# Performance work log

Measured on AMD Instinct MI355X. Metric: run time of the kernel, lower is better.

The kernel has to match this reference:

```python
import jax, jax.numpy as jnp
import numpy as np

HIDDEN = 1024
MOE_INTER = 512
SHARED_INTER = 2048
N_EXPERTS = 32
TOP_K = 6
N_GROUP = 8
TOPK_GROUP = 4
ROUTED_SCALE = 2.5


def setup_inputs() -> dict:
    key = jax.random.key(0)
    ks = jax.random.split(key, 6)
    s = 0.02
    return {
        "hidden_states": jax.random.normal(ks[0], (2, 1024, HIDDEN), jnp.float32),
        "gate_w": jax.random.normal(ks[1], (N_EXPERTS, HIDDEN), jnp.float32) * s,
        "e_bias": jnp.zeros((N_EXPERTS,), jnp.float32),  # e_score_correction_bias (non-trainable)
        "up_w": jax.random.normal(ks[2], (N_EXPERTS, MOE_INTER, HIDDEN), jnp.float32) * s,
        "down_w": jax.random.normal(ks[3], (N_EXPERTS, HIDDEN, MOE_INTER), jnp.float32) * s,
        "shared_up_w": jax.random.normal(ks[4], (SHARED_INTER, HIDDEN), jnp.float32) * s,
        "shared_down_w": jax.random.normal(ks[5], (HIDDEN, SHARED_INTER), jnp.float32) * s,
    }


def _relu2(x):
    # Nemotron-H 'relu2' activation: relu(x)^2
    return jnp.square(jax.nn.relu(x))


def _router(x, gate_w, e_bias):
    # x: [T, H] -> topk_idx [T, K] (int), topk_w [T, K] (fp32)
    T = x.shape[0]
    logits = x.astype(jnp.float32) @ gate_w.astype(jnp.float32).T  # [T, E]
    scores = jax.nn.sigmoid(logits)
    sc = scores + e_bias[None, :]
    # group-limited routing: top-2 sum per group, keep topk_group groups
    g = sc.reshape(T, N_GROUP, N_EXPERTS // N_GROUP)
    group_scores = jax.lax.top_k(g, 2)[0].sum(-1)                  # [T, G]
    group_idx = jax.lax.top_k(group_scores, TOPK_GROUP)[1]         # [T, TG]
    group_mask = jnp.zeros_like(group_scores).at[jnp.arange(T)[:, None], group_idx].set(1.0)
    score_mask = jnp.repeat(group_mask, N_EXPERTS // N_GROUP, axis=1)  # [T, E]
    masked = jnp.where(score_mask > 0, sc, 0.0)
    topk_idx = jax.lax.stop_gradient(jax.lax.top_k(masked, TOP_K)[1])  # torch path is @no_grad
    topk_w = jnp.take_along_axis(scores, topk_idx, axis=1)         # gather from unbiased scores
    topk_w = topk_w / (topk_w.sum(-1, keepdims=True) + 1e-20)      # norm_topk_prob
    topk_w = topk_w * ROUTED_SCALE
    return topk_idx, topk_w


def reference(hidden_states, gate_w, e_bias, up_w, down_w, shared_up_w, shared_down_w):
    B, S, H = hidden_states.shape
    x = hidden_states.reshape(-1, H)  # [T, H]
    T = x.shape[0]
    topk_idx, topk_w = _router(x, gate_w, e_bias)
    # combine weights as dense [T, E] (scatter of top-k weights)
    combine = jnp.zeros((T, N_EXPERTS), topk_w.dtype).at[jnp.arange(T)[:, None], topk_idx].add(topk_w)
    # dense-masked expert compute; weight applied on intermediate (equivalent since
    # down_proj is linear with no bias): out = sum_e w_te * down_e(act(up_e(x)))
    h = _relu2(jnp.einsum('th,eih->tei', x, up_w))   # [T, E, I]
    h = h * combine[:, :, None]
    moe_out = jnp.einsum('tei,ehi->th', h, down_w)   # [T, H]
    shared = _relu2(x @ shared_up_w.T) @ shared_down_w.T
    return (moe_out + shared).reshape(B, S, H)


if __name__ == "__main__":
    out = reference(**setup_inputs())
    print(out.shape, out.dtype)
```

## Files before the change

### kernel.cpp

```cpp
#include <hip/hip_runtime.h>

typedef unsigned short u16;
typedef __bf16 bf16x8 __attribute__((ext_vector_type(8)));
typedef float f32x4 __attribute__((ext_vector_type(4)));

#define T_TOK 2048
#define HID   1024
#define NEXP  32
#define IM    512
#define SI    2048
#define TOPK  6
#define PLAN_MAX 160

__device__ __forceinline__ u16 f2bf(float f){
  unsigned u = __float_as_uint(f);
  u += 0x7FFFu + ((u >> 16) & 1u);
  return (u16)(u >> 16);
}

__device__ __forceinline__ void gll16(const void* g, void* l){
  __builtin_amdgcn_global_load_lds((const __attribute__((address_space(1))) void*)g,
                                   (__attribute__((address_space(3))) void*)l, 16, 0, 0);
}

__global__ __launch_bounds__(256) void cvt_all_kernel(const float4* __restrict__ s0,
                                                      const float4* __restrict__ s1,
                                                      const float4* __restrict__ s2,
                                                      const float4* __restrict__ s3,
                                                      const float4* __restrict__ s4,
                                                      ushort4* __restrict__ d0,
                                                      ushort4* __restrict__ d1,
                                                      ushort4* __restrict__ d2,
                                                      ushort4* __restrict__ d3,
                                                      ushort4* __restrict__ d4){
  long i = (long)blockIdx.x * 256 + threadIdx.x;
  const float4* s; ushort4* d;
  if      (i <  524288L)                 { s = s0;            d = d0;            }
  else if (i <  524288L + 4194304L)      { s = s1 - 524288L;  d = d1 - 524288L;  }
  else if (i <  524288L + 8388608L)      { s = s2 - 4718592L; d = d2 - 4718592L; }
  else if (i <  524288L + 8912896L)      { s = s3 - 8912896L; d = d3 - 8912896L; }
  else                                   { s = s4 - 9437184L; d = d4 - 9437184L; }
  float4 v = s[i];
  ushort4 o; o.x = f2bf(v.x); o.y = f2bf(v.y); o.z = f2bf(v.z); o.w = f2bf(v.w);
  d[i] = o;
}

__global__ __launch_bounds__(256) void router_kernel(const float* __restrict__ x,
                                                     const float* __restrict__ gate,
                                                     const float* __restrict__ ebias,
                                                     int* __restrict__ ce,
                                                     float* __restrict__ cw){
  int wave = threadIdx.x >> 6;
  int lane = threadIdx.x & 63;
  int t = blockIdx.x * 4 + wave;
  int e = lane & 31, half = lane >> 5;
  const float4* xv = (const float4*)(x + (size_t)t * HID);
  const float4* gv = (const float4*)(gate + (size_t)e * HID);
  double d0 = 0, d1 = 0, d2 = 0, d3 = 0;
  for (int i = half * 128; i < half * 128 + 128; i++){
    float4 a = xv[i], b = gv[i];
    d0 += (double)a.x * b.x; d1 += (double)a.y * b.y;
    d2 += (double)a.z * b.z; d3 += (double)a.w * b.w;
  }
  double acc = (d0 + d1) + (d2 + d3);
  acc += __shfl_xor(acc, 32);
  double score = 1.0 / (1.0 + exp(-acc));
  double sc = score + (double)ebias[e];
  double o1  = __shfl_xor(sc, 1);
  double hi  = fmax(sc, o1), lo = fmin(sc, o1);
  double ohi = __shfl_xor(hi, 2), olo = __shfl_xor(lo, 2);
  double gs  = (hi >= ohi) ? hi + fmax(lo, ohi) : ohi + fmax(olo, hi);
  int g = e >> 2;
  int rank = 0;
#pragma unroll
  for (int j = 0; j < 8; j++){
    double gj = __shfl(gs, j * 4);
    if (gj > gs || (gj == gs && j < g)) rank++;
  }
  double cur = (rank < 4) ? sc : 0.0;
  int sel_e[TOPK]; double sel_w[TOPK]; double wsum = 0.0;
#pragma unroll
  for (int k = 0; k < TOPK; k++){
    double bv = cur; int bi = lane;
#pragma unroll
    for (int m = 32; m >= 1; m >>= 1){
      double ov = __shfl_xor(bv, m); int oi = __shfl_xor(bi, m);
      if (ov > bv || (ov == bv && oi < bi)) { bv = ov; bi = oi; }
    }
    if ((bi & 31) == e) cur = -1e300;
    double ws = __shfl(score, bi);
    sel_e[k] = bi; sel_w[k] = ws; wsum += ws;
  }
  double scale = 2.5 / (wsum + 1e-20);
#pragma unroll
  for (int k = 0; k < TOPK; k++){
    if (lane == k){
      ce[t * TOPK + k] = sel_e[k] & 31;
      cw[t * TOPK + k] = (float)(sel_w[k] * scale);
    }
  }
}

__global__ __launch_bounds__(256) void build_kernel(const int* __restrict__ ce,
                                                    const float* __restrict__ cw,
                                                    int* __restrict__ cnt,
                                                    int* __restrict__ tok,
                                                    float* __restrict__ wl){
  int e = blockIdx.x;
  int tid = threadIdx.x, lane = tid & 63, wave = tid >> 6;
  __shared__ int wsum[4];
  int running = 0;
  for (int base = 0; base < T_TOK * TOPK; base += 256){
    int i = base + tid;
    bool m = (ce[i] == e);
    unsigned long long bal = __ballot(m);
    int woff = __popcll(bal & ((1ull << lane) - 1ull));
    if (lane == 0) wsum[wave] = __popcll(bal);
    __syncthreads();
    int wbase = 0;
#pragma unroll
    for (int wv = 0; wv < 4; wv++) if (wv < wave) wbase += wsum[wv];
    int btot = wsum[0] + wsum[1] + wsum[2] + wsum[3];
    if (m){
      int t = i / TOPK, k = i - t * TOPK;
      int pos = running + wbase + woff;
      tok[e * T_TOK + pos] = (t << 3) | k;
      wl[e * T_TOK + pos] = cw[i];
    }
    running += btot;
    __syncthreads();
  }
  if (tid == 0) cnt[e] = running;
}

__global__ __launch_bounds__(256) void plan_kernel(const int* __restrict__ cnt,
                                                   int* __restrict__ plan){
  int tid = threadIdx.x;
  if (tid < PLAN_MAX) plan[1 + tid] = -1;
  __syncthreads();
  if (tid == 0){
    int n = 0;
    for (int e = 0; e < NEXP; e++){
      int c = cnt[e];
      for (int tb = 0; tb < c; tb += 128) plan[1 + n++] = (tb << 8) | e;
    }
    plan[0] = n;
  }
}

__device__ __forceinline__ void gemm_core(
    const char* gA0, const char* gA1, const char* gB0, const char* gB1,
    u16* lA, u16* lB, int iters, int tid, int wrow, int wcol, int quad, int l16,
    f32x4 acc[4][4])
{
  char* dA0 = (char*)lA + tid*16;
  char* dA1 = (char*)lA + 4096 + tid*16;
  char* dB0 = (char*)lB + tid*16;
  char* dB1 = (char*)lB + 4096 + tid*16;
  for (int it = 0; it < iters; ++it){
    gll16(gA0, dA0); gll16(gA1, dA1);
    gll16(gB0, dB0); gll16(gB1, dB1);
    gA0 += 64; gA1 += 64; gB0 += 64; gB1 += 64;
    __syncthreads();
    bf16x8 af[4], bfr[4];
#pragma unroll
    for (int mt = 0; mt < 4; mt++) af[mt] = *(const bf16x8*)&lA[(wrow + mt*16 + l16)*32 + quad*8];
#pragma unroll
    for (int nt = 0; nt < 4; nt++) bfr[nt] = *(const bf16x8*)&lB[(wcol + nt*16 + l16)*32 + quad*8];
#pragma unroll
    for (int mt = 0; mt < 4; mt++)
#pragma unroll
      for (int nt = 0; nt < 4; nt++)
        acc[mt][nt] = __builtin_amdgcn_mfma_f32_16x16x32_bf16(af[mt], bfr[nt], acc[mt][nt], 0, 0, 0);
    __syncthreads();
  }
}

#define ACC_INIT f32x4 acc[4][4]; \
  _Pragma("unroll") for (int i_ = 0; i_ < 4; i_++) \
  _Pragma("unroll") for (int j_ = 0; j_ < 4; j_++) acc[i_][j_] = (f32x4){0.f,0.f,0.f,0.f};

__global__ __launch_bounds__(256) void sh_up_kernel(const u16* __restrict__ A,
                                                    const u16* __restrict__ B,
                                                    u16* __restrict__ C){
  __shared__ u16 lA[128*32], lB[128*32];
  int tid = threadIdx.x;
  int bm = blockIdx.x*128, bn = blockIdx.y*128;
  int lane = tid & 63, wave = tid >> 6, quad = lane >> 4, l16 = lane & 15;
  int wrow = (wave >> 1)*64, wcol = (wave & 1)*64;
  int srow = tid >> 2, sseg = (tid & 3)*16;
  const char* gA0 = (const char*)(A + (size_t)(bm + srow)*HID) + sseg;
  const char* gA1 = (const char*)(A + (size_t)(bm + 64 + srow)*HID) + sseg;
  const char* gB0 = (const char*)(B + (size_t)(bn + srow)*HID) + sseg;
  const char* gB1 = (const char*)(B + (size_t)(bn + 64 + srow)*HID) + sseg;
  ACC_INIT;
  gemm_core(gA0, gA1, gB0, gB1, lA, lB, HID/32, tid, wrow, wcol, quad, l16, acc);
#pragma unroll
  for (int mt = 0; mt < 4; mt++)
#pragma unroll
    for (int nt = 0; nt < 4; nt++)
#pragma unroll
      for (int r = 0; r < 4; r++){
        int m = bm + wrow + mt*16 + quad*4 + r;
        int n = bn + wcol + nt*16 + l16;
        float v = acc[mt][nt][r]; v = fmaxf(v, 0.f); v *= v;
        C[(size_t)m*SI + n] = f2bf(v);
      }
}

__global__ __launch_bounds__(256) void sh_down_kernel(const u16* __restrict__ A,
                                                      const u16* __restrict__ B,
                                                      float* __restrict__ C){
  __shared__ u16 lA[128*32], lB[128*32];
  int tid = threadIdx.x;
  int bm = blockIdx.x*128, bn = blockIdx.y*128;
  int lane = tid & 63, wave = tid >> 6, quad = lane >> 4, l16 = lane & 15;
  int wrow = (wave >> 1)*64, wcol = (wave & 1)*64;
  int srow = tid >> 2, sseg = (tid & 3)*16;
  const char* gA0 = (const char*)(A + (size_t)(bm + srow)*SI) + sseg;
  const char* gA1 = (const char*)(A + (size_t)(bm + 64 + srow)*SI) + sseg;
  const char* gB0 = (const char*)(B + (size_t)(bn + srow)*SI) + sseg;
  const char* gB1 = (const char*)(B + (size_t)(bn + 64 + srow)*SI) + sseg;
  ACC_INIT;
  gemm_core(gA0, gA1, gB0, gB1, lA, lB, SI/32, tid, wrow, wcol, quad, l16, acc);
#pragma unroll
  for (int mt = 0; mt < 4; mt++)
#pragma unroll
    for (int nt = 0; nt < 4; nt++)
#pragma unroll
      for (int r = 0; r < 4; r++){
        int m = bm + wrow + mt*16 + quad*4 + r;
        int n = bn + wcol + nt*16 + l16;
        C[(size_t)m*HID + n] = acc[mt][nt][r];
      }
}

__global__ __launch_bounds__(256) void expert_up_kernel(const u16* __restrict__ xb,
                                                        const u16* __restrict__ upb,
                                                        const int* __restrict__ cnt,
                                                        const int* __restrict__ tok,
                                                        const float* __restrict__ wl,
                                                        const int* __restrict__ plan,
                                                        u16* __restrict__ hws){
  int pv = plan[1 + blockIdx.x];
  if (pv < 0) return;
  int e = pv & 255;
  int tb = pv >> 8;
  int c = cnt[e];
  int bn = blockIdx.y * 128;
  const int* tl = tok + e * T_TOK;
  const float* wle = wl + e * T_TOK;
  __shared__ u16 lA[128*32], lB[128*32];
  int tid = threadIdx.x;
  int lane = tid & 63, wave = tid >> 6, quad = lane >> 4, l16 = lane & 15;
  int wrow = (wave >> 1)*64, wcol = (wave & 1)*64;
  int srow = tid >> 2, sseg = (tid & 3)*16;
  int s0 = tb + srow;      if (s0 > c-1) s0 = c-1;
  int s1 = tb + 64 + srow; if (s1 > c-1) s1 = c-1;
  int t0 = tl[s0] >> 3, t1 = tl[s1] >> 3;
  const char* gA0 = (const char*)(xb + (size_t)t0*HID) + sseg;
  const char* gA1 = (const char*)(xb + (size_t)t1*HID) + sseg;
  const u16* Bb = upb + (size_t)e * IM * HID;
  const char* gB0 = (const char*)(Bb + (size_t)(bn + srow)*HID) + sseg;
  const char* gB1 = (const char*)(Bb + (size_t)(bn + 64 + srow)*HID) + sseg;
  ACC_INIT;
  gemm_core(gA0, gA1, gB0, gB1, lA, lB, HID/32, tid, wrow, wcol, quad, l16, acc);
#pragma unroll
  for (int mt = 0; mt < 4; mt++)
#pragma unroll
    for (int r = 0; r < 4; r++){
      int s = tb + wrow + mt*16 + quad*4 + r;
      if (s < c){
        int code = tl[s];
        float w = wle[s];
        size_t hb = ((size_t)(code >> 3) * TOPK + (code & 7)) * IM;
#pragma unroll
        for (int nt = 0; nt < 4; nt++){
          float v = acc[mt][nt][r]; v = fmaxf(v, 0.f); v = v * v * w;
          hws[hb + bn + wcol + nt*16 + l16] = f2bf(v);
        }
      }
    }
}

__global__ __launch_bounds__(256) void expert_down_kernel(const u16* __restrict__ hws,
                                                          const u16* __restrict__ dnb,
                                                          const int* __restrict__ cnt,
                                                          const int* __restrict__ tok,
                                                          const int* __restrict__ plan,
                                                          float* __restrict__ dws){
  int pv = plan[1 + blockIdx.x];
  if (pv < 0) return;
  int e = pv & 255;
  int tb = pv >> 8;
  int c = cnt[e];
  int bn = blockIdx.y * 128;
  const int* tl = tok + e * T_TOK;
  __shared__ u16 lA[128*32], lB[128*32];
  int tid = threadIdx.x;
  int lane = tid & 63, wave = tid >> 6, quad = lane >> 4, l16 = lane & 15;
  int wrow = (wave >> 1)*64, wcol = (wave & 1)*64;
  int srow = tid >> 2, sseg = (tid & 3)*16;
  int s0 = tb + srow;      if (s0 > c-1) s0 = c-1;
  int s1 = tb + 64 + srow; if (s1 > c-1) s1 = c-1;
  int c0 = tl[s0], c1 = tl[s1];
  const char* gA0 = (const char*)(hws + ((size_t)(c0 >> 3)*TOPK + (c0 & 7))*IM) + sseg;
  const char* gA1 = (const char*)(hws + ((size_t)(c1 >> 3)*TOPK + (c1 & 7))*IM) + sseg;
  const u16* Bb = dnb + (size_t)e * HID * IM;
  const char* gB0 = (const char*)(Bb + (size_t)(bn + srow)*IM) + sseg;
  const char* gB1 = (const char*)(Bb + (size_t)(bn + 64 + srow)*IM) + sseg;
  ACC_INIT;
  gemm_core(gA0, gA1, gB0, gB1, lA, lB, IM/32, tid, wrow, wcol, quad, l16, acc);
#pragma unroll
  for (int mt = 0; mt < 4; mt++)
#pragma unroll
    for (int r = 0; r < 4; r++){
      int s = tb + wrow + mt*16 + quad*4 + r;
      if (s < c){
        int code = tl[s];
        size_t db = ((size_t)(code >> 3) * TOPK + (code & 7)) * HID;
#pragma unroll
        for (int nt = 0; nt < 4; nt++)
          dws[db + bn + wcol + nt*16 + l16] = acc[mt][nt][r];
      }
    }
}

__global__ __launch_bounds__(256) void reduce_kernel(const float4* __restrict__ dws,
                                                     float4* __restrict__ out){
  int i = blockIdx.x * 256 + threadIdx.x;
  int t = i >> 8;
  int col = i & 255;
  const float4* p = dws + (size_t)t * TOPK * 256 + col;
  float4 s = out[i];
#pragma unroll
  for (int k = 0; k < TOPK; k++){
    float4 v = p[(size_t)k * 256];
    s.x += v.x; s.y += v.y; s.z += v.z; s.w += v.w;
  }
  out[i] = s;
}

extern "C" void kernel_launch(void* const* d_in, const int* in_sizes, int n_in,
                              void* d_out, int out_size, void* d_ws, size_t ws_size,
                              hipStream_t stream) {
  const float* x    = (const float*)d_in[0];
  const float* gate = (const float*)d_in[1];
  const float* eb   = (const float*)d_in[2];
  const float* upw  = (const float*)d_in[3];
  const float* dnw  = (const float*)d_in[4];
  const float* supw = (const float*)d_in[5];
  const float* sdnw = (const float*)d_in[6];
  float* out = (float*)d_out;

  char* w = (char*)d_ws;
  size_t o = 0;
  int*   cnt  = (int*)(w + o);   o += 1024;
  int*   plan = (int*)(w + o);   o += 1024;
  int*   ce   = (int*)(w + o);   o += (size_t)T_TOK * TOPK * 4;
  float* cw   = (float*)(w + o); o += (size_t)T_TOK * TOPK * 4;
  int*   tok  = (int*)(w + o);   o += (size_t)NEXP * T_TOK * 4;
  float* wl   = (float*)(w + o); o += (size_t)NEXP * T_TOK * 4;
  u16*   xb   = (u16*)(w + o);   o += (size_t)T_TOK * HID * 2;
  u16*   dnb  = (u16*)(w + o);   o += (size_t)NEXP * HID * IM * 2;
  u16*   hws  = (u16*)(w + o);   o += (size_t)T_TOK * TOPK * IM * 2;
  size_t region = o;
  u16*   upb  = (u16*)(w + o);   o += (size_t)NEXP * IM * HID * 2;
  u16*   supb = (u16*)(w + o);   o += (size_t)SI * HID * 2;
  u16*   sdnb = (u16*)(w + o);   o += (size_t)HID * SI * 2;
  u16*   shh  = (u16*)(w + o);   o += (size_t)T_TOK * SI * 2;
  float* dws  = (float*)(w + region);

  cvt_all_kernel<<<9961472 / 256, 256, 0, stream>>>(
      (const float4*)x, (const float4*)upw, (const float4*)dnw,
      (const float4*)supw, (const float4*)sdnw,
      (ushort4*)xb, (ushort4*)upb, (ushort4*)dnb, (ushort4*)supb, (ushort4*)sdnb);

  router_kernel<<<T_TOK/4, 256, 0, stream>>>(x, gate, eb, ce, cw);
  build_kernel<<<NEXP, 256, 0, stream>>>(ce, cw, cnt, tok, wl);
  plan_kernel<<<1, 256, 0, stream>>>(cnt, plan);

  sh_up_kernel<<<dim3(T_TOK/128, SI/128), 256, 0, stream>>>(xb, supb, shh);
  sh_down_kernel<<<dim3(T_TOK/128, HID/128), 256, 0, stream>>>(shh, sdnb, out);

  expert_up_kernel<<<dim3(PLAN_MAX, IM/128), 256, 0, stream>>>(xb, upb, cnt, tok, wl, plan, hws);
  expert_down_kernel<<<dim3(PLAN_MAX, HID/128), 256, 0, stream>>>(hws, dnb, cnt, tok, plan, dws);

  reduce_kernel<<<(T_TOK * HID / 4) / 256, 256, 0, stream>>>((const float4*)dws, (float4*)out);
}
```

Measured before the change: 393.4 us.

## Fuse top-k reduction into expert down GEMM via atomics; widen bf16 conversion

```diff
diff --git a/kernel.cpp b/kernel.cpp
--- a/kernel.cpp
+++ b/kernel.cpp
@@ -3,6 +3,7 @@
 typedef unsigned short u16;
 typedef __bf16 bf16x8 __attribute__((ext_vector_type(8)));
 typedef float f32x4 __attribute__((ext_vector_type(4)));
+typedef u16 u16x8 __attribute__((ext_vector_type(8)));
 
 #define T_TOK 2048
 #define HID   1024
@@ -23,26 +24,38 @@
                                    (__attribute__((address_space(3))) void*)l, 16, 0, 0);
 }
 
-__global__ __launch_bounds__(256) void cvt_all_kernel(const float4* __restrict__ s0,
-                                                      const float4* __restrict__ s1,
+__device__ __forceinline__ u16x8 cvt2(float4 a, float4 b){
+  u16x8 o;
+  o[0] = f2bf(a.x); o[1] = f2bf(a.y); o[2] = f2bf(a.z); o[3] = f2bf(a.w);
+  o[4] = f2bf(b.x); o[5] = f2bf(b.y); o[6] = f2bf(b.z); o[7] = f2bf(b.w);
+  return o;
+}
+
+__global__ __launch_bounds__(256) void cvt_big_kernel(const float4* __restrict__ s1,
                                                       const float4* __restrict__ s2,
-                                                      const float4* __restrict__ s3,
-                                                      const float4* __restrict__ s4,
-                                                      ushort4* __restrict__ d0,
-                                                      ushort4* __restrict__ d1,
-                                                      ushort4* __restrict__ d2,
-                                                      ushort4* __restrict__ d3,
-                                                      ushort4* __restrict__ d4){
+                                                      u16x8* __restrict__ d1,
+                                                      u16x8* __restrict__ d2){
   long i = (long)blockIdx.x * 256 + threadIdx.x;
-  const float4* s; ushort4* d;
-  if      (i <  524288L)                 { s = s0;            d = d0;            }
-  else if (i <  524288L + 4194304L)      { s = s1 - 524288L;  d = d1 - 524288L;  }
-  else if (i <  524288L + 8388608L)      { s = s2 - 4718592L; d = d2 - 4718592L; }
-  else if (i <  524288L + 8912896L)      { s = s3 - 8912896L; d = d3 - 8912896L; }
-  else                                   { s = s4 - 9437184L; d = d4 - 9437184L; }
-  float4 v = s[i];
-  ushort4 o; o.x = f2bf(v.x); o.y = f2bf(v.y); o.z = f2bf(v.z); o.w = f2bf(v.w);
-  d[i] = o;
+  const float4* s; u16x8* d;
+  if (i < 2097152L){ s = s1; d = d1; }
+  else             { s = s2; d = d2; i -= 2097152L; }
+  float4 a = s[2*i], b = s[2*i+1];
+  d[i] = cvt2(a, b);
+}
+
+__global__ __launch_bounds__(256) void cvt_small_kernel(const float4* __restrict__ s0,
+                                                        const float4* __restrict__ s3,
+                                                        const float4* __restrict__ s4,
+                                                        u16x8* __restrict__ d0,
+                                                        u16x8* __restrict__ d3,
+                                                        u16x8* __restrict__ d4){
+  long i = (long)blockIdx.x * 256 + threadIdx.x;
+  const float4* s; u16x8* d;
+  if      (i < 262144L){ s = s0; d = d0; }
+  else if (i < 524288L){ s = s3; d = d3; i -= 262144L; }
+  else                 { s = s4; d = d4; i -= 524288L; }
+  float4 a = s[2*i], b = s[2*i+1];
+  d[i] = cvt2(a, b);
 }
 
 __global__ __launch_bounds__(256) void router_kernel(const float* __restrict__ x,
@@ -288,7 +301,7 @@
                                                           const int* __restrict__ cnt,
                                                           const int* __restrict__ tok,
                                                           const int* __restrict__ plan,
-                                                          float* __restrict__ dws){
+                                                          float* __restrict__ out){
   int pv = plan[1 + blockIdx.x];
   if (pv < 0) return;
   int e = pv & 255;
@@ -318,27 +331,12 @@
       int s = tb + wrow + mt*16 + quad*4 + r;
       if (s < c){
         int code = tl[s];
-        size_t db = ((size_t)(code >> 3) * TOPK + (code & 7)) * HID;
+        float* ob = out + (size_t)(code >> 3) * HID;
 #pragma unroll
         for (int nt = 0; nt < 4; nt++)
-          dws[db + bn + wcol + nt*16 + l16] = acc[mt][nt][r];
+          unsafeAtomicAdd(&ob[bn + wcol + nt*16 + l16], acc[mt][nt][r]);
       }
     }
-}
-
-__global__ __launch_bounds__(256) void reduce_kernel(const float4* __restrict__ dws,
-                                                     float4* __restrict__ out){
-  int i = blockIdx.x * 256 + threadIdx.x;
-  int t = i >> 8;
-  int col = i & 255;
-  const float4* p = dws + (size_t)t * TOPK * 256 + col;
-  float4 s = out[i];
-#pragma unroll
-  for (int k = 0; k < TOPK; k++){
-    float4 v = p[(size_t)k * 256];
-    s.x += v.x; s.y += v.y; s.z += v.z; s.w += v.w;
-  }
-  out[i] = s;
 }
 
 extern "C" void kernel_launch(void* const* d_in, const int* in_sizes, int n_in,
@@ -364,17 +362,16 @@
   u16*   xb   = (u16*)(w + o);   o += (size_t)T_TOK * HID * 2;
   u16*   dnb  = (u16*)(w + o);   o += (size_t)NEXP * HID * IM * 2;
   u16*   hws  = (u16*)(w + o);   o += (size_t)T_TOK * TOPK * IM * 2;
-  size_t region = o;
   u16*   upb  = (u16*)(w + o);   o += (size_t)NEXP * IM * HID * 2;
   u16*   supb = (u16*)(w + o);   o += (size_t)SI * HID * 2;
   u16*   sdnb = (u16*)(w + o);   o += (size_t)HID * SI * 2;
   u16*   shh  = (u16*)(w + o);   o += (size_t)T_TOK * SI * 2;
-  float* dws  = (float*)(w + region);
-
-  cvt_all_kernel<<<9961472 / 256, 256, 0, stream>>>(
-      (const float4*)x, (const float4*)upw, (const float4*)dnw,
-      (const float4*)supw, (const float4*)sdnw,
-      (ushort4*)xb, (ushort4*)upb, (ushort4*)dnb, (ushort4*)supb, (ushort4*)sdnb);
+
+  cvt_big_kernel<<<16384, 256, 0, stream>>>(
+      (const float4*)upw, (const float4*)dnw, (u16x8*)upb, (u16x8*)dnb);
+  cvt_small_kernel<<<3072, 256, 0, stream>>>(
+      (const float4*)x, (const float4*)supw, (const float4*)sdnw,
+      (u16x8*)xb, (u16x8*)supb, (u16x8*)sdnb);
 
   router_kernel<<<T_TOK/4, 256, 0, stream>>>(x, gate, eb, ce, cw);
   build_kernel<<<NEXP, 256, 0, stream>>>(ce, cw, cnt, tok, wl);
@@ -384,7 +381,5 @@
   sh_down_kernel<<<dim3(T_TOK/128, HID/128), 256, 0, stream>>>(shh, sdnb, out);
 
   expert_up_kernel<<<dim3(PLAN_MAX, IM/128), 256, 0, stream>>>(xb, upb, cnt, tok, wl, plan, hws);
-  expert_down_kernel<<<dim3(PLAN_MAX, HID/128), 256, 0, stream>>>(hws, dnb, cnt, tok, plan, dws);
-
-  reduce_kernel<<<(T_TOK * HID / 4) / 256, 256, 0, stream>>>((const float4*)dws, (float4*)out);
-}
+  expert_down_kernel<<<dim3(PLAN_MAX, HID/128), 256, 0, stream>>>(hws, dnb, cnt, tok, plan, out);
+}
```

After: 407.2 us. +3.5%, slower.
